# Kernel tuning notes

Measured on AMD Instinct MI355X. Metric: run time of the kernel, lower is better.

Reference implementation:

```python
import jax, jax.numpy as jnp
import numpy as np

B, L, D_MODEL = 4, 2048, 2048
N_HEADS, HEAD_DIM = 16, 128
EPS = 1e-6


def _make_rope(key_unused, L, dim, base=10000.0):
    inv_freq = 1.0 / (base ** (np.arange(0, dim, 2, dtype=np.float32) / dim))  # [dim/2]
    t = np.arange(L, dtype=np.float32)
    freqs = np.outer(t, inv_freq)  # [L, dim/2]
    emb = np.concatenate([freqs, freqs], axis=-1)  # [L, dim]
    cos = np.broadcast_to(np.cos(emb)[None], (B, L, dim)).copy()
    sin = np.broadcast_to(np.sin(emb)[None], (B, L, dim)).copy()
    return jnp.asarray(cos), jnp.asarray(sin)


def setup_inputs() -> dict:
    key = jax.random.key(0)
    ks = jax.random.split(key, 8)
    s = 1.0 / np.sqrt(D_MODEL)
    x = jax.random.normal(ks[0], (B, L, D_MODEL), dtype=jnp.float32)
    cos_q, sin_q = _make_rope(None, L, HEAD_DIM)
    cos_k, sin_k = _make_rope(None, L, HEAD_DIM)
    Wq = jax.random.normal(ks[1], (D_MODEL, D_MODEL), dtype=jnp.float32) * s
    Wk = jax.random.normal(ks[2], (D_MODEL, D_MODEL), dtype=jnp.float32) * s
    Wv = jax.random.normal(ks[3], (D_MODEL, D_MODEL), dtype=jnp.float32) * s
    Wo = jax.random.normal(ks[4], (D_MODEL, D_MODEL), dtype=jnp.float32) * s
    q_gamma = jnp.ones((HEAD_DIM,), dtype=jnp.float32) + 0.02 * jax.random.normal(ks[5], (HEAD_DIM,), dtype=jnp.float32)
    k_gamma = jnp.ones((HEAD_DIM,), dtype=jnp.float32) + 0.02 * jax.random.normal(ks[6], (HEAD_DIM,), dtype=jnp.float32)
    return dict(x=x, cos_q=cos_q, sin_q=sin_q, cos_k=cos_k, sin_k=sin_k,
                Wq=Wq, Wk=Wk, Wv=Wv, Wo=Wo, q_gamma=q_gamma, k_gamma=k_gamma)


def _rms_norm(h, w):
    # T5-style RMSNorm over last dim (head_dim), variance in fp32
    var = jnp.mean(h.astype(jnp.float32) ** 2, axis=-1, keepdims=True)
    return w * (h * jax.lax.rsqrt(var + EPS))


def _rotate_half(x):
    d = x.shape[-1] // 2
    return jnp.concatenate([-x[..., d:], x[..., :d]], axis=-1)


def _apply_rope(x, cos, sin):
    # x: [B, L, H, Dh]; cos/sin: [B, L, Dh] -> broadcast over heads
    c = cos[:, :, None, :]
    s = sin[:, :, None, :]
    return x * c + _rotate_half(x) * s


def reference(x, cos_q, sin_q, cos_k, sin_k, Wq, Wk, Wv, Wo, q_gamma, k_gamma):
    Bx, Lx, _ = x.shape
    # QKV projections (Linear with weight [out, in]: y = x @ W.T)
    q = (x @ Wq.T).reshape(Bx, Lx, N_HEADS, HEAD_DIM)
    k = (x @ Wk.T).reshape(Bx, Lx, N_HEADS, HEAD_DIM)
    v = (x @ Wv.T).reshape(Bx, Lx, N_HEADS, HEAD_DIM)
    # per-head QK RMSNorm
    q = _rms_norm(q, q_gamma)
    k = _rms_norm(k, k_gamma)
    # dual RoPE
    q = _apply_rope(q, cos_q, sin_q)
    k = _apply_rope(k, cos_k, sin_k)
    # scaled dot-product attention (dense, no mask)
    scale = 1.0 / jnp.sqrt(jnp.asarray(HEAD_DIM, dtype=x.dtype))
    scores = jnp.einsum('blhd,bmhd->bhlm', q, k) * scale
    attn = jax.nn.softmax(scores, axis=-1)
    out = jnp.einsum('bhlm,bmhd->blhd', attn, v)
    out = out.reshape(Bx, Lx, N_HEADS * HEAD_DIM)
    return out @ Wo.T
```

## Files before the change

kernel.cpp:

```cpp
#include <hip/hip_runtime.h>
#include <stdint.h>

#define DM   2048
#define LSEQ 2048
#define NB   4
#define NH   16
#define HD   128
#define BL   (NB*LSEQ)
#define NK64 (DM/32)

typedef unsigned short u16;
typedef short  short8  __attribute__((ext_vector_type(8)));
typedef short  short4v __attribute__((ext_vector_type(4)));
typedef float  f32x4   __attribute__((ext_vector_type(4)));
typedef float  f32x16  __attribute__((ext_vector_type(16)));

#define LOG2E 1.4426950408889634f

__device__ __forceinline__ float bf2f(u16 v) {
    union { unsigned u; float f; } x; x.u = ((unsigned)v) << 16; return x.f;
}
__device__ __forceinline__ u16 f2bf(float f) {
    union { float f; unsigned u; } x; x.f = f;
    return (u16)((x.u + 0x7FFF + ((x.u >> 16) & 1)) >> 16);
}

__device__ __forceinline__ short8 ld8(const void* base, size_t e, bool f32) {
    if (f32) {
        const float* p = (const float*)base + e;
        f32x4 a = *(const f32x4*)p;
        f32x4 b = *(const f32x4*)(p + 4);
        short8 r;
        #pragma unroll
        for (int i = 0; i < 4; ++i) { r[i] = (short)f2bf(a[i]); r[4+i] = (short)f2bf(b[i]); }
        return r;
    }
    return *(const short8*)((const u16*)base + e);
}
__device__ __forceinline__ float lde(const void* b, size_t e, bool f32) {
    return f32 ? ((const float*)b)[e] : bf2f(((const u16*)b)[e]);
}
__device__ __forceinline__ void st1(void* b, size_t e, float v, bool f32) {
    if (f32) ((float*)b)[e] = v; else ((u16*)b)[e] = f2bf(v);
}

extern "C" __global__ void dtype_probe(const u16* __restrict__ x, int* __restrict__ cnt) {
    int t = threadIdx.x;
    int insane = 0;
    #pragma unroll
    for (int j = 0; j < 16; ++j) {
        u16 u = x[t * 16 + j];
        int e = (u >> 7) & 0xFF;
        if (u != 0 && (e < 96 || e > 143)) insane++;
    }
    atomicAdd(cnt, insane);
}

extern "C" __global__ void to_bf16(const void* __restrict__ in, u16* __restrict__ out,
                                   int n8, const int* __restrict__ cnt)
{
    const bool isf = *cnt > 100;
    int i = blockIdx.x * 256 + threadIdx.x;
    if (i >= n8) return;
    *(short8*)(out + (size_t)i * 8) = ld8(in, (size_t)i * 8, isf);
}

extern "C" __global__ void to_bf16_w(const void* w0, const void* w1,
                                     const void* w2, const void* w3,
                                     u16* o0, u16* o1, u16* o2, u16* o3,
                                     int n8, const int* __restrict__ cnt)
{
    const bool isf = *cnt > 100;
    int i = blockIdx.x * 256 + threadIdx.x;
    if (i >= n8) return;
    const void* in; u16* out;
    switch (blockIdx.y) {
        case 0:  in = w0; out = o0; break;
        case 1:  in = w1; out = o1; break;
        case 2:  in = w2; out = o2; break;
        default: in = w3; out = o3; break;
    }
    *(short8*)(out + (size_t)i * 8) = ld8(in, (size_t)i * 8, isf);
}

__device__ __forceinline__ int swz128(int row, int col) {
    return row*128 + ((((col >> 3) ^ row) & 15) << 3) + (col & 7);
}
__device__ __forceinline__ int swz64(int row, int col) {
    return row*64 + ((((col >> 3) ^ row) & 7) << 3) + (col & 7);
}

__device__ __forceinline__ void xcd_swz8(int& bx, int& by, int& bz) {
    const int lin = blockIdx.x + (blockIdx.y << 3) + (blockIdx.z << 8);
    const int nq  = (gridDim.z << 8) >> 3;
    const int nid = (lin & 7) * nq + (lin >> 3);
    bx = nid & 7; by = (nid >> 3) & 31; bz = nid >> 8;
}

typedef __attribute__((address_space(1))) const unsigned int guint;
typedef __attribute__((address_space(3))) unsigned int luint;
__device__ __forceinline__ void gl_lds16(const void* g, void* l) {
    __builtin_amdgcn_global_load_lds((guint*)g, (luint*)l, 16, 0, 0);
}

__device__ __forceinline__ void g256_stage(const u16* ag, const u16* wg,
                                           u16* buf, int k0, int wofs)
{
    gl_lds16(ag + k0,                    buf + wofs);
    gl_lds16(ag + k0 + (size_t)128 * DM, buf + 4096 + wofs);
    gl_lds16(wg + k0,                    buf + 8192 + wofs);
    gl_lds16(wg + k0 + (size_t)128 * DM, buf + 12288 + wofs);
}

__device__ __forceinline__ void g256_core(const u16* __restrict__ A,
                                          const u16* __restrict__ W,
                                          u16* lds, f32x4 acc[8][4],
                                          int m0, int n0, int t)
{
    const int lane = t & 63, w = t >> 6;
    const int quad = lane >> 4, l15 = lane & 15;
    const int wr = (w >> 2) * 128, wc = (w & 3) * 64;
    const int srow = t >> 2, scol = (t & 3) * 8;
    const u16* ag = A + (size_t)(m0 + srow) * DM + scol;
    const u16* wg = W + (size_t)(n0 + srow) * DM + scol;
    const int wofs = w * 512;

    #pragma unroll
    for (int i = 0; i < 8; ++i)
        #pragma unroll
        for (int j = 0; j < 4; ++j) acc[i][j] = (f32x4){0.f, 0.f, 0.f, 0.f};

    g256_stage(ag, wg, lds,          0, wofs);
    g256_stage(ag, wg, lds + 16384, 32, wofs);
    asm volatile("s_waitcnt vmcnt(4)" ::: "memory");
    __builtin_amdgcn_sched_barrier(0);
    __builtin_amdgcn_s_barrier();
    __builtin_amdgcn_sched_barrier(0);

    int cur = 0, nx2 = 2;
    for (int kt = 0; kt < NK64; ++kt) {
        if (kt + 2 < NK64)
            g256_stage(ag, wg, lds + nx2 * 16384, (kt + 2) * 32, wofs);
        const u16* Ab = lds + cur * 16384;
        const u16* Bb = Ab + 8192;
        short8 afr[8], bfr[4];
        #pragma unroll
        for (int nt = 0; nt < 4; ++nt)
            bfr[nt] = *(const short8*)&Bb[(wc + nt*16 + l15)*32 + quad*8];
        #pragma unroll
        for (int mt = 0; mt < 8; ++mt)
            afr[mt] = *(const short8*)&Ab[(wr + mt*16 + l15)*32 + quad*8];
        __builtin_amdgcn_s_setprio(1);
        #pragma unroll
        for (int mt = 0; mt < 8; ++mt)
            #pragma unroll
            for (int nt = 0; nt < 4; ++nt)
                acc[mt][nt] = __builtin_amdgcn_mfma_f32_16x16x32_bf16(
                                  afr[mt], bfr[nt], acc[mt][nt], 0, 0, 0);
        __builtin_amdgcn_s_setprio(0);
        if (kt + 2 < NK64) asm volatile("s_waitcnt vmcnt(4)" ::: "memory");
        else               asm volatile("s_waitcnt vmcnt(0)" ::: "memory");
        __builtin_amdgcn_sched_barrier(0);
        __builtin_amdgcn_s_barrier();
        __builtin_amdgcn_sched_barrier(0);
        cur = (cur == 2) ? 0 : cur + 1;
        nx2 = (nx2 == 2) ? 0 : nx2 + 1;
    }
}

extern "C" __global__ __launch_bounds__(512, 2) void gemm256_bf(
    const u16* __restrict__ A, const u16* __restrict__ W,
    void* __restrict__ O, const int* __restrict__ cnt, int o_sel)
{
    __shared__ __align__(16) u16 lds[49152];
    const bool of = o_sel && (*cnt > 100);
    int bx, by, bz;  xcd_swz8(bx, by, bz);
    const int n0 = bx * 256, m0 = by * 256;
    const int t = threadIdx.x, lane = t & 63;
    const int quad = lane >> 4, l15 = lane & 15;
    const int wr = ((t >> 6) >> 2) * 128, wc = ((t >> 6) & 3) * 64;

    f32x4 acc[8][4];
    g256_core(A, W, lds, acc, m0, n0, t);

    #pragma unroll
    for (int mt = 0; mt < 8; ++mt)
        #pragma unroll
        for (int r = 0; r < 4; ++r) {
            size_t base = (size_t)(m0 + wr + mt*16 + quad*4 + r) * DM + n0 + wc + l15;
            #pragma unroll
            for (int nt = 0; nt < 4; ++nt) st1(O, base + nt*16, acc[mt][nt][r], of);
        }
}

extern "C" __global__ __launch_bounds__(512, 2) void gemm256_qk2(
    const u16* __restrict__ A, const u16* __restrict__ W0, const u16* __restrict__ W1,
    u16* __restrict__ O0, u16* __restrict__ O1)
{
    __shared__ __align__(16) u16 lds[49152];
    int bx, by, bz;  xcd_swz8(bx, by, bz);
    const u16* W = bz ? W1 : W0;
    u16*       O = bz ? O1 : O0;
    const int n0 = bx * 256, m0 = by * 256;
    const int t = threadIdx.x, lane = t & 63;
    const int quad = lane >> 4, l15 = lane & 15;
    const int wr = ((t >> 6) >> 2) * 128, wc = ((t >> 6) & 3) * 64;

    f32x4 acc[8][4];
    g256_core(A, W, lds, acc, m0, n0, t);

    #pragma unroll
    for (int mt = 0; mt < 8; ++mt)
        #pragma unroll
        for (int r = 0; r < 4; ++r) {
            size_t base = (size_t)(m0 + wr + mt*16 + quad*4 + r) * DM + n0 + wc + l15;
            #pragma unroll
            for (int nt = 0; nt < 4; ++nt) O[base + nt*16] = f2bf(acc[mt][nt][r]);
        }
}

extern "C" __global__ __launch_bounds__(512, 2) void gemm256_vb(
    const u16* __restrict__ A, const u16* __restrict__ W, u16* __restrict__ vT)
{
    __shared__ __align__(16) u16 lds[49152];
    int bx, by, bz;  xcd_swz8(bx, by, bz);
    const int n0 = bx * 256, m0 = by * 256;
    const int t = threadIdx.x, lane = t & 63;
    const int quad = lane >> 4, l15 = lane & 15;
    const int wr = ((t >> 6) >> 2) * 128, wc = ((t >> 6) & 3) * 64;

    f32x4 acc[8][4];
    g256_core(A, W, lds, acc, m0, n0, t);

    const int b  = m0 >> 11;
    const int l0 = (m0 & (LSEQ - 1)) + wr + quad*4;
    #pragma unroll
    for (int mt = 0; mt < 8; ++mt)
        #pragma unroll
        for (int nt = 0; nt < 4; ++nt) {
            short4v sv;
            #pragma unroll
            for (int r = 0; r < 4; ++r) sv[r] = (short)f2bf(acc[mt][nt][r]);
            int n = n0 + wc + nt*16 + l15;
            *(short4v*)(vT + (size_t)b*DM*LSEQ + (size_t)n*LSEQ + l0 + mt*16) = sv;
        }
}

extern "C" __global__ void rmsrope(u16* __restrict__ q, u16* __restrict__ kk,
    const void* cq, const void* sq, const void* ck, const void* sk,
    const void* qg, const void* kg, const int* cnt)
{
    const bool isf = *cnt > 100;
    const float slc = 0.08838834764831845f * LOG2E;
    int t = blockIdx.x * 256 + threadIdx.x;
    int lane = t & 63;
    int widx = t >> 6;
    int h  = widx & (NH - 1);
    int bl = widx >> 4;
    size_t ro = (size_t)bl * DM + (size_t)h * HD;
    size_t co = (size_t)bl * HD;

    {
        float e0 = bf2f(q[ro + lane]), e1 = bf2f(q[ro + lane + 64]);
        float ss = e0*e0 + e1*e1;
        #pragma unroll
        for (int sm = 1; sm < 64; sm <<= 1) ss += __shfl_xor(ss, sm, 64);
        float r = rsqrtf(ss * (1.f / HD) + 1e-6f);
        float y0 = e0 * r * lde(qg, lane, isf);
        float y1 = e1 * r * lde(qg, lane + 64, isf);
        float c0 = lde(cq, co + lane, isf), c1 = lde(cq, co + lane + 64, isf);
        float s0 = lde(sq, co + lane, isf), s1 = lde(sq, co + lane + 64, isf);
        q[ro + lane]      = f2bf((y0 * c0 - y1 * s0) * slc);
        q[ro + lane + 64] = f2bf((y1 * c1 + y0 * s1) * slc);
    }
    {
        float e0 = bf2f(kk[ro + lane]), e1 = bf2f(kk[ro + lane + 64]);
        float ss = e0*e0 + e1*e1;
        #pragma unroll
        for (int sm = 1; sm < 64; sm <<= 1) ss += __shfl_xor(ss, sm, 64);
        float r = rsqrtf(ss * (1.f / HD) + 1e-6f);
        float y0 = e0 * r * lde(kg, lane, isf);
        float y1 = e1 * r * lde(kg, lane + 64, isf);
        float c0 = lde(ck, co + lane, isf), c1 = lde(ck, co + lane + 64, isf);
        float s0 = lde(sk, co + lane, isf), s1 = lde(sk, co + lane + 64, isf);
        kk[ro + lane]      = f2bf(y0 * c0 - y1 * s0);
        kk[ro + lane + 64] = f2bf(y1 * c1 + y0 * s1);
    }
}

extern "C" __global__ __launch_bounds__(256, 2) void flash(
    const u16* q, const u16* __restrict__ k,
    const u16* __restrict__ vT, u16* o)
{
    __shared__ __align__(16) u16 lds[32768];

    const int bh = blockIdx.x, b = bh >> 4, h = bh & 15;
    const int q0 = blockIdx.y * 128;
    const int t = threadIdx.x, lane = t & 63, w = t >> 6;
    const int l31 = lane & 31, hi8 = (lane >> 5) * 8;
    const size_t qko = (size_t)b * LSEQ * DM + (size_t)h * HD;
    const size_t vo  = (size_t)b * DM * LSEQ + (size_t)h * HD * LSEQ;

    short8 qf[8];
    #pragma unroll
    for (int ks = 0; ks < 8; ++ks)
        qf[ks] = *(const short8*)(q + qko +
                  (size_t)(q0 + w*32 + l31) * DM + ks*16 + hi8);

    f32x16 zz;
    #pragma unroll
    for (int r = 0; r < 16; ++r) zz[r] = 0.f;
    f32x16 acc[4];
    f32x16 dacc;
    #pragma unroll
    for (int dt = 0; dt < 4; ++dt) acc[dt] = zz;
    dacc = zz;

    const short onev = (l31 == 0) ? (short)0x3F80 : (short)0;
    const short8 onesA = {onev, onev, onev, onev, onev, onev, onev, onev};

    const int krow = t >> 4,  kc8 = (t & 15) * 8;
    const int vrow = t >> 3,  vc8 = (t & 7) * 8;
    short8 kreg[4], vreg[4];

    #pragma unroll
    for (int it = 0; it < 4; ++it) {
        kreg[it] = *(const short8*)(k  + qko + (size_t)(krow + it*16) * DM + kc8);
        vreg[it] = *(const short8*)(vT + vo  + (size_t)(vrow + it*32) * LSEQ + vc8);
    }
    {
        u16* Kn = lds;  u16* Vn = lds + 8192;
        #pragma unroll
        for (int it = 0; it < 4; ++it) {
            *(short8*)&Kn[swz128(krow + it*16, kc8)] = kreg[it];
            *(short8*)&Vn[swz64 (vrow + it*32, vc8)] = vreg[it];
        }
    }
    #pragma unroll
    for (int it = 0; it < 4; ++it) {
        kreg[it] = *(const short8*)(k  + qko + (size_t)(64 + krow + it*16) * DM + kc8);
        vreg[it] = *(const short8*)(vT + vo  + (size_t)(vrow + it*32) * LSEQ + 64 + vc8);
    }
    __syncthreads();

    const int NT = LSEQ / 64;
    for (int it0 = 0; it0 < NT; ++it0) {
        const int cur = it0 & 1;
        if (it0 + 1 < NT) {
            u16* Kn = lds + (cur ^ 1) * 16384;
            u16* Vn = Kn + 8192;
            #pragma unroll
            for (int it = 0; it < 4; ++it) {
                *(short8*)&Kn[swz128(krow + it*16, kc8)] = kreg[it];
                *(short8*)&Vn[swz64 (vrow + it*32, vc8)] = vreg[it];
            }
        }
        if (it0 + 2 < NT) {
            const int kv = (it0 + 2) * 64;
            #pragma unroll
            for (int it = 0; it < 4; ++it) {
                kreg[it] = *(const short8*)(k  + qko + (size_t)(kv + krow + it*16) * DM + kc8);
                vreg[it] = *(const short8*)(vT + vo  + (size_t)(vrow + it*32) * LSEQ + kv + vc8);
            }
        }
        u16* Kl = lds + cur * 16384;
        u16* Vl = Kl + 8192;

        f32x16 S0, S1;
        __builtin_amdgcn_s_setprio(1);
        {
            short8 kf0 = *(const short8*)&Kl[swz128(l31,      hi8)];
            short8 kf1 = *(const short8*)&Kl[swz128(32 + l31, hi8)];
            S0 = __builtin_amdgcn_mfma_f32_32x32x16_bf16(kf0, qf[0], zz, 0, 0, 0);
            S1 = __builtin_amdgcn_mfma_f32_32x32x16_bf16(kf1, qf[0], zz, 0, 0, 0);
        }
        #pragma unroll
        for (int ks = 1; ks < 8; ++ks) {
            short8 kf0 = *(const short8*)&Kl[swz128(l31,      ks*16 + hi8)];
            short8 kf1 = *(const short8*)&Kl[swz128(32 + l31, ks*16 + hi8)];
            S0 = __builtin_amdgcn_mfma_f32_32x32x16_bf16(kf0, qf[ks], S0, 0, 0, 0);
            S1 = __builtin_amdgcn_mfma_f32_32x32x16_bf16(kf1, qf[ks], S1, 0, 0, 0);
        }
        __builtin_amdgcn_s_setprio(0);

        float p[32];
        #pragma unroll
        for (int r = 0; r < 16; ++r) p[r]      = exp2f(S0[r]);
        #pragma unroll
        for (int r = 0; r < 16; ++r) p[16 + r] = exp2f(S1[r]);

        #pragma unroll
        for (int kt = 0; kt < 2; ++kt) {
            unsigned pk[8];
            #pragma unroll
            for (int j = 0; j < 8; ++j)
                asm("v_cvt_pk_bf16_f32 %0, %1, %2"
                    : "=v"(pk[j]) : "v"(p[kt*16 + 2*j]), "v"(p[kt*16 + 2*j + 1]));
            asm volatile("v_permlane32_swap_b32 %0, %1" : "+v"(pk[0]), "+v"(pk[2]));
            asm volatile("v_permlane32_swap_b32 %0, %1" : "+v"(pk[1]), "+v"(pk[3]));
            asm volatile("v_permlane32_swap_b32 %0, %1" : "+v"(pk[4]), "+v"(pk[6]));
            asm volatile("v_permlane32_swap_b32 %0, %1" : "+v"(pk[5]), "+v"(pk[7]));
            union { unsigned u[4]; short8 v; } f0, f1;
            f0.u[0] = pk[0]; f0.u[1] = pk[1]; f0.u[2] = pk[2]; f0.u[3] = pk[3];
            f1.u[0] = pk[4]; f1.u[1] = pk[5]; f1.u[2] = pk[6]; f1.u[3] = pk[7];
            #pragma unroll
            for (int s = 0; s < 2; ++s) {
                short8 pf = s ? f1.v : f0.v;
                int slice = kt*2 + s;
                __builtin_amdgcn_s_setprio(1);
                #pragma unroll
                for (int dt = 0; dt < 4; ++dt) {
                    short8 vf = *(const short8*)&Vl[swz64(dt*32 + l31, slice*16 + hi8)];
                    acc[dt] = __builtin_amdgcn_mfma_f32_32x32x16_bf16(vf, pf, acc[dt], 0, 0, 0);
                }
                dacc = __builtin_amdgcn_mfma_f32_32x32x16_bf16(onesA, pf, dacc, 0, 0, 0);
                __builtin_amdgcn_s_setprio(0);
            }
        }
        __syncthreads();
    }

    u16* Ol = lds + w * 4352;
    float dn0 = dacc[0];
    float dnx = __shfl_xor(dn0, 32, 64);
    float inv = 1.f / ((lane & 32) ? dnx : dn0);
    #pragma unroll
    for (int dt = 0; dt < 4; ++dt)
        #pragma unroll
        for (int i = 0; i < 8; ++i) {
            float a0 = acc[dt][2*i]     * inv;
            float a1 = acc[dt][2*i + 1] * inv;
            unsigned pkv;
            asm("v_cvt_pk_bf16_f32 %0, %1, %2" : "=v"(pkv) : "v"(a0), "v"(a1));
            int d = dt*32 + ((i & 1) << 1) + ((i >> 1) << 3) + ((lane >> 5) << 2);
            *(unsigned*)&Ol[l31*136 + d] = pkv;
        }
    __syncthreads();
    #pragma unroll
    for (int j = 0; j < 8; ++j) {
        int cb = (lane >> 5) + 2*j;
        short8 vv = *(const short8*)&Ol[l31*136 + cb*8];
        *(short8*)(o + qko + (size_t)(q0 + w*32 + l31) * DM + cb*8) = vv;
    }
}

extern "C" void kernel_launch(void* const* d_in, const int* in_sizes, int n_in,
                              void* d_out, int out_size, void* d_ws, size_t ws_size,
                              hipStream_t stream)
{
    const void* x  = d_in[0];
    const void* cq = d_in[1];
    const void* sq = d_in[2];
    const void* ck = d_in[3];
    const void* sk = d_in[4];
    const void* Wq = d_in[5];
    const void* Wk = d_in[6];
    const void* Wv = d_in[7];
    const void* Wo = d_in[8];
    const void* qg = d_in[9];
    const void* kg = d_in[10];

    u16* qws = (u16*)d_ws;
    u16* kws = qws + (size_t)BL * DM;
    u16* vtw = kws + (size_t)BL * DM;
    u16* wqs = vtw + (size_t)BL * DM;
    u16* wks = wqs + (size_t)DM * DM;
    u16* wvs = wks + (size_t)DM * DM;
    u16* wos = wvs + (size_t)DM * DM;
    int* cnt = (int*)(wos + (size_t)DM * DM);
    u16* xb  = (u16*)d_out;

    const int xn8 = BL * DM / 8;
    const int wn8 = DM * DM / 8;

    hipMemsetAsync(cnt, 0, 4, stream);
    dtype_probe<<<1, 256, 0, stream>>>((const u16*)x, cnt);

    to_bf16<<<xn8 / 256, 256, 0, stream>>>(x, xb, xn8, cnt);
    to_bf16_w<<<dim3(wn8 / 256, 4), 256, 0, stream>>>(Wq, Wk, Wv, Wo,
                                                      wqs, wks, wvs, wos, wn8, cnt);

    gemm256_vb <<<dim3(8, 32),    512, 0, stream>>>(xb, wvs, vtw);
    gemm256_qk2<<<dim3(8, 32, 2), 512, 0, stream>>>(xb, wqs, wks, qws, kws);

    rmsrope<<<dim3(BL * NH / 4), 256, 0, stream>>>(qws, kws, cq, sq, ck, sk, qg, kg, cnt);

    flash<<<dim3(64, 16), 256, 0, stream>>>(qws, kws, vtw, qws);

    gemm256_bf<<<dim3(8, 32), 512, 0, stream>>>(qws, wos, d_out, cnt, 1);
}
```

Before: 684.2 us.

## Swizzle GEMM LDS layout, merge Q/K/V projections, relax flash loop barriers

The GEMM staging now rotates each thread's 16-byte column chunk by row and reads fragments with a matching rotated offset, to cut LDS bank conflicts on the fragment loads. The separate V-projection and Q/K-projection launches are merged into one 3-slice grid, removing a launch and the tail between the two kernels. In the flash loop, the per-iteration __syncthreads is replaced by an explicit lgkmcnt wait plus barrier, with a vmcnt(0) wait placed before the register-to-LDS stores. The swizzle must match exactly on the store and load sides, and the new wait placement changes how global prefetch overlaps with compute.

```diff
diff --git a/kernel.cpp b/kernel.cpp
--- a/kernel.cpp
+++ b/kernel.cpp
@@ -24,6 +24,13 @@
     union { float f; unsigned u; } x; x.f = f;
     return (u16)((x.u + 0x7FFF + ((x.u >> 16) & 1)) >> 16);
 }
+
+#define BAR_LGKM() do {                                        \
+    asm volatile("s_waitcnt lgkmcnt(0)" ::: "memory");         \
+    __builtin_amdgcn_sched_barrier(0);                         \
+    __builtin_amdgcn_s_barrier();                              \
+    __builtin_amdgcn_sched_barrier(0);                         \
+} while (0)
 
 __device__ __forceinline__ short8 ld8(const void* base, size_t e, bool f32) {
     if (f32) {
@@ -120,10 +127,12 @@
     const int lane = t & 63, w = t >> 6;
     const int quad = lane >> 4, l15 = lane & 15;
     const int wr = (w >> 2) * 128, wc = (w & 3) * 64;
-    const int srow = t >> 2, scol = (t & 3) * 8;
+    const int srow = t >> 2;
+    const int scol = ((((t & 3) - (t >> 3)) & 3) << 3);
     const u16* ag = A + (size_t)(m0 + srow) * DM + scol;
     const u16* wg = W + (size_t)(n0 + srow) * DM + scol;
     const int wofs = w * 512;
+    const int rq = (((quad + (l15 >> 1)) & 3) << 3);
 
     #pragma unroll
     for (int i = 0; i < 8; ++i)
@@ -146,10 +155,10 @@
         short8 afr[8], bfr[4];
         #pragma unroll
         for (int nt = 0; nt < 4; ++nt)
-            bfr[nt] = *(const short8*)&Bb[(wc + nt*16 + l15)*32 + quad*8];
+            bfr[nt] = *(const short8*)&Bb[(wc + nt*16 + l15)*32 + rq];
         #pragma unroll
         for (int mt = 0; mt < 8; ++mt)
-            afr[mt] = *(const short8*)&Ab[(wr + mt*16 + l15)*32 + quad*8];
+            afr[mt] = *(const short8*)&Ab[(wr + mt*16 + l15)*32 + rq];
         __builtin_amdgcn_s_setprio(1);
         #pragma unroll
         for (int mt = 0; mt < 8; ++mt)
@@ -193,14 +202,14 @@
         }
 }
 
-extern "C" __global__ __launch_bounds__(512, 2) void gemm256_qk2(
-    const u16* __restrict__ A, const u16* __restrict__ W0, const u16* __restrict__ W1,
-    u16* __restrict__ O0, u16* __restrict__ O1)
+extern "C" __global__ __launch_bounds__(512, 2) void gemm256_proj(
+    const u16* __restrict__ A,
+    const u16* __restrict__ Wq, const u16* __restrict__ Wk, const u16* __restrict__ Wv,
+    u16* __restrict__ Oq, u16* __restrict__ Ok, u16* __restrict__ vT)
 {
     __shared__ __align__(16) u16 lds[49152];
     int bx, by, bz;  xcd_swz8(bx, by, bz);
-    const u16* W = bz ? W1 : W0;
-    u16*       O = bz ? O1 : O0;
+    const u16* W = (bz == 0) ? Wv : (bz == 1 ? Wq : Wk);
     const int n0 = bx * 256, m0 = by * 256;
     const int t = threadIdx.x, lane = t & 63;
     const int quad = lane >> 4, l15 = lane & 15;
@@ -209,41 +218,30 @@
     f32x4 acc[8][4];
     g256_core(A, W, lds, acc, m0, n0, t);
 
-    #pragma unroll
-    for (int mt = 0; mt < 8; ++mt)
-        #pragma unroll
-        for (int r = 0; r < 4; ++r) {
-            size_t base = (size_t)(m0 + wr + mt*16 + quad*4 + r) * DM + n0 + wc + l15;
-            #pragma unroll
-            for (int nt = 0; nt < 4; ++nt) O[base + nt*16] = f2bf(acc[mt][nt][r]);
-        }
-}
-
-extern "C" __global__ __launch_bounds__(512, 2) void gemm256_vb(
-    const u16* __restrict__ A, const u16* __restrict__ W, u16* __restrict__ vT)
-{
-    __shared__ __align__(16) u16 lds[49152];
-    int bx, by, bz;  xcd_swz8(bx, by, bz);
-    const int n0 = bx * 256, m0 = by * 256;
-    const int t = threadIdx.x, lane = t & 63;
-    const int quad = lane >> 4, l15 = lane & 15;
-    const int wr = ((t >> 6) >> 2) * 128, wc = ((t >> 6) & 3) * 64;
-
-    f32x4 acc[8][4];
-    g256_core(A, W, lds, acc, m0, n0, t);
-
-    const int b  = m0 >> 11;
-    const int l0 = (m0 & (LSEQ - 1)) + wr + quad*4;
-    #pragma unroll
-    for (int mt = 0; mt < 8; ++mt)
-        #pragma unroll
-        for (int nt = 0; nt < 4; ++nt) {
-            short4v sv;
-            #pragma unroll
-            for (int r = 0; r < 4; ++r) sv[r] = (short)f2bf(acc[mt][nt][r]);
-            int n = n0 + wc + nt*16 + l15;
-            *(short4v*)(vT + (size_t)b*DM*LSEQ + (size_t)n*LSEQ + l0 + mt*16) = sv;
-        }
+    if (bz == 0) {
+        const int b  = m0 >> 11;
+        const int l0 = (m0 & (LSEQ - 1)) + wr + quad*4;
+        #pragma unroll
+        for (int mt = 0; mt < 8; ++mt)
+            #pragma unroll
+            for (int nt = 0; nt < 4; ++nt) {
+                short4v sv;
+                #pragma unroll
+                for (int r = 0; r < 4; ++r) sv[r] = (short)f2bf(acc[mt][nt][r]);
+                int n = n0 + wc + nt*16 + l15;
+                *(short4v*)(vT + (size_t)b*DM*LSEQ + (size_t)n*LSEQ + l0 + mt*16) = sv;
+            }
+    } else {
+        u16* O = (bz == 1) ? Oq : Ok;
+        #pragma unroll
+        for (int mt = 0; mt < 8; ++mt)
+            #pragma unroll
+            for (int r = 0; r < 4; ++r) {
+                size_t base = (size_t)(m0 + wr + mt*16 + quad*4 + r) * DM + n0 + wc + l15;
+                #pragma unroll
+                for (int nt = 0; nt < 4; ++nt) O[base + nt*16] = f2bf(acc[mt][nt][r]);
+            }
+    }
 }
 
 extern "C" __global__ void rmsrope(u16* __restrict__ q, u16* __restrict__ kk,
@@ -347,6 +345,8 @@
     for (int it0 = 0; it0 < NT; ++it0) {
         const int cur = it0 & 1;
         if (it0 + 1 < NT) {
+            asm volatile("s_waitcnt vmcnt(0)" ::: "memory");
+            __builtin_amdgcn_sched_barrier(0);
             u16* Kn = lds + (cur ^ 1) * 16384;
             u16* Vn = Kn + 8192;
             #pragma unroll
@@ -417,9 +417,10 @@
                 __builtin_amdgcn_s_setprio(0);
             }
         }
-        __syncthreads();
-    }
-
+        BAR_LGKM();
+    }
+
+    __syncthreads();
     u16* Ol = lds + w * 4352;
     float dn0 = dacc[0];
     float dnx = __shfl_xor(dn0, 32, 64);
@@ -480,8 +481,8 @@
     to_bf16_w<<<dim3(wn8 / 256, 4), 256, 0, stream>>>(Wq, Wk, Wv, Wo,
                                                       wqs, wks, wvs, wos, wn8, cnt);
 
-    gemm256_vb <<<dim3(8, 32),    512, 0, stream>>>(xb, wvs, vtw);
-    gemm256_qk2<<<dim3(8, 32, 2), 512, 0, stream>>>(xb, wqs, wks, qws, kws);
+    gemm256_proj<<<dim3(8, 32, 3), 512, 0, stream>>>(xb, wqs, wks, wvs,
+                                                     qws, kws, vtw);
 
     rmsrope<<<dim3(BL * NH / 4), 256, 0, stream>>>(qws, kws, cq, sq, ck, sk, qg, kg, cnt);
 
```

New measurement: 678.5 us. Within noise of the previous version (-0.8%).
